# Performance work log

Measured on AMD Instinct MI355X. Metric: run time of the kernel, lower is better.

Reference implementation:

```python
import jax, jax.numpy as jnp
import numpy as np

D_MODEL = 1024
NUM_HEADS = 16
D_K = D_MODEL // NUM_HEADS


def setup_inputs() -> dict:
    key = jax.random.key(0)
    ks = jax.random.split(key, 11)
    B, S = 4, 2048
    s = 1.0 / np.sqrt(D_MODEL)
    return {
        "q": jax.random.normal(ks[0], (B, S, D_MODEL), jnp.float32),
        "k": jax.random.normal(ks[1], (B, S, D_MODEL), jnp.float32),
        "v": jax.random.normal(ks[2], (B, S, D_MODEL), jnp.float32),
        "w_q": jax.random.normal(ks[3], (D_MODEL, D_MODEL), jnp.float32) * s,
        "b_q": jnp.zeros((D_MODEL,), jnp.float32),
        "w_k": jax.random.normal(ks[4], (D_MODEL, D_MODEL), jnp.float32) * s,
        "b_k": jnp.zeros((D_MODEL,), jnp.float32),
        "w_v": jax.random.normal(ks[5], (D_MODEL, D_MODEL), jnp.float32) * s,
        "b_v": jnp.zeros((D_MODEL,), jnp.float32),
        "w_o": jax.random.normal(ks[6], (D_MODEL, D_MODEL), jnp.float32) * s,
        "b_o": jnp.zeros((D_MODEL,), jnp.float32),
    }


def reference(q, k, v, w_q, b_q, w_k, b_k, w_v, b_v, w_o, b_o):
    B, S, _ = q.shape
    # projections; torch Linear computes x @ W.T + b
    def proj(x, w, b):
        y = x @ w.T + b
        return y.reshape(B, -1, NUM_HEADS, D_K).transpose(0, 2, 1, 3)  # (B,H,S,d_k)

    qh, kh, vh = proj(q, w_q, b_q), proj(k, w_k, b_k), proj(v, w_v, b_v)
    scores = jnp.einsum("bhqd,bhkd->bhqk", qh, kh) / jnp.sqrt(jnp.float32(D_K))
    attn_weights = jax.nn.softmax(scores, axis=-1)
    x = jnp.einsum("bhqk,bhkd->bhqd", attn_weights, vh)
    x = x.transpose(0, 2, 1, 3).reshape(B, -1, D_MODEL)
    out = x @ w_o.T + b_o
    return out, attn_weights
```

## Files before the change

### kernel.cpp

```cpp
#include <hip/hip_runtime.h>
#include <math.h>

#define S_LEN 2048
#define DM 1024
#define NH 16
#define DK 64

typedef __attribute__((ext_vector_type(8))) short short8;
typedef __attribute__((ext_vector_type(4))) short short4v;
typedef __attribute__((ext_vector_type(4))) float f32x4;

#define LGKM_BARRIER() do { \
    asm volatile("s_waitcnt lgkmcnt(0)" ::: "memory"); \
    __builtin_amdgcn_s_barrier(); \
    __builtin_amdgcn_sched_barrier(0); \
  } while (0)

__device__ __forceinline__ short f2bf(float f) {
  unsigned u = __builtin_bit_cast(unsigned, f);
  u = (u + 0x7FFFu + ((u >> 16) & 1u)) >> 16;
  return (short)u;
}

__device__ __forceinline__ void gld_lds16(const short* g, short* l) {
  __builtin_amdgcn_global_load_lds(
      (const __attribute__((address_space(1))) unsigned int*)g,
      (__attribute__((address_space(3))) unsigned int*)l, 16, 0, 0);
}

__global__ __launch_bounds__(256) void cvt_bf16(
    const float* __restrict__ s0, const float* __restrict__ s1,
    const float* __restrict__ s2, const float* __restrict__ s3,
    short* __restrict__ d0, short* __restrict__ d1,
    short* __restrict__ d2, short* __restrict__ d3, int n)
{
  const float* s; short* d;
  switch (blockIdx.y) {
    case 0:  s = s0; d = d0; break;
    case 1:  s = s1; d = d1; break;
    case 2:  s = s2; d = d2; break;
    default: s = s3; d = d3; break;
  }
  const int i = (blockIdx.x * 256 + threadIdx.x) * 8;
  if (i < n) {
    const float4 v0 = *(const float4*)&s[i];
    const float4 v1 = *(const float4*)&s[i + 4];
    short8 r = { f2bf(v0.x), f2bf(v0.y), f2bf(v0.z), f2bf(v0.w),
                 f2bf(v1.x), f2bf(v1.y), f2bf(v1.z), f2bf(v1.w) };
    *(short8*)&d[i] = r;
  }
}

__global__ __launch_bounds__(256) void proj3(
    const short* __restrict__ qb, const short* __restrict__ kb, const short* __restrict__ vb,
    const short* __restrict__ wqb, const short* __restrict__ wkb, const short* __restrict__ wvb,
    const float* __restrict__ biq, const float* __restrict__ bik, const float* __restrict__ biv,
    short* __restrict__ qhb, short* __restrict__ khb, short* __restrict__ vtb)
{
  __shared__ short SM[17408];
  short* As = SM;
  short* Bs = SM + 4096;

  const int z = blockIdx.z;
  const short* A; const short* B; const float* bias; short* o;
  if (z == 0)      { A = qb; B = wqb; bias = biq; o = qhb; }
  else if (z == 1) { A = kb; B = wkb; bias = bik; o = khb; }
  else             { A = vb; B = wvb; bias = biv; o = vtb; }

  const int tid = threadIdx.x;
  const int lane = tid & 63;
  const int wv = tid >> 6;
  const int grp = lane >> 4, lid = lane & 15;
  const int wr = wv >> 1, wc = wv & 1;
  const int bm = blockIdx.x, bn = blockIdx.y;

  f32x4 acc[4][4] = {};

  const int idx0 = tid, idx1 = 256 + tid;
  const int r0 = idx0 >> 2, c0 = (idx0 & 3) * 8;
  const int r1 = idx1 >> 2, c1 = (idx1 & 3) * 8;
  const short* a0 = &A[(size_t)(bm * 128 + r0) * DM + c0];
  const short* a1 = &A[(size_t)(bm * 128 + r1) * DM + c1];
  const short* b0 = &B[(size_t)(bn * 128 + r0) * DM + c0];
  const short* b1 = &B[(size_t)(bn * 128 + r1) * DM + c1];

  for (int ks = 0; ks < 32; ++ks) {
    __syncthreads();
    gld_lds16(a0 + ks * 32, &As[idx0 * 8]);
    gld_lds16(a1 + ks * 32, &As[idx1 * 8]);
    gld_lds16(b0 + ks * 32, &Bs[idx0 * 8]);
    gld_lds16(b1 + ks * 32, &Bs[idx1 * 8]);
    __syncthreads();
    short8 a[4], b[4];
    #pragma unroll
    for (int m = 0; m < 4; ++m) a[m] = *(const short8*)&As[(wr * 64 + m * 16 + lid) * 32 + grp * 8];
    #pragma unroll
    for (int n = 0; n < 4; ++n) b[n] = *(const short8*)&Bs[(wc * 64 + n * 16 + lid) * 32 + grp * 8];
    #pragma unroll
    for (int m = 0; m < 4; ++m)
      #pragma unroll
      for (int n = 0; n < 4; ++n)
        acc[m][n] = __builtin_amdgcn_mfma_f32_16x16x32_bf16(a[m], b[n], acc[m][n], 0, 0, 0);
  }

  if (z < 2) {
    #pragma unroll
    for (int n = 0; n < 4; ++n) {
      const int ng = bn * 128 + wc * 64 + n * 16 + lid;
      const float bvs = bias[ng];
      const int h = ng >> 6, d = ng & 63;
      #pragma unroll
      for (int m = 0; m < 4; ++m) {
        const int mg = bm * 128 + wr * 64 + m * 16 + grp * 4;
        const int bb = mg >> 11, s = mg & 2047;
        #pragma unroll
        for (int r = 0; r < 4; ++r)
          o[(((size_t)bb * NH + h) * S_LEN + s + r) * DK + d] = f2bf(acc[m][n][r] + bvs);
      }
    }
  } else {
    __syncthreads();
    #pragma unroll
    for (int n = 0; n < 4; ++n) {
      const int ngl = wc * 64 + n * 16 + lid;
      const float bvs = bias[bn * 128 + ngl];
      #pragma unroll
      for (int m = 0; m < 4; ++m) {
        const int sl = wr * 64 + m * 16 + grp * 4;
        short4v c4 = { f2bf(acc[m][n][0] + bvs), f2bf(acc[m][n][1] + bvs),
                       f2bf(acc[m][n][2] + bvs), f2bf(acc[m][n][3] + bvs) };
        *(short4v*)&SM[ngl * 136 + sl] = c4;
      }
    }
    __syncthreads();
    const int bb = bm >> 4, s0 = (bm & 15) * 128;
    #pragma unroll
    for (int i = 0; i < 8; ++i) {
      const int id = tid + 256 * i;
      const int row = id >> 4;
      const int c8 = (id & 15) * 8;
      const short8 vv = *(const short8*)&SM[row * 136 + c8];
      *(short8*)&o[((size_t)bb * 1024 + bn * 128 + row) * S_LEN + s0 + c8] = vv;
    }
  }
}

__global__ __launch_bounds__(256) void gemm_o(
    const short* __restrict__ A, const short* __restrict__ B,
    const float* __restrict__ bias, float* __restrict__ of)
{
  __shared__ short As[128 * 32];
  __shared__ short Bs[128 * 32];
  const int tid = threadIdx.x;
  const int lane = tid & 63;
  const int wv = tid >> 6;
  const int grp = lane >> 4, lid = lane & 15;
  const int wr = wv >> 1, wc = wv & 1;
  const int bm = blockIdx.x, bn = blockIdx.y;

  f32x4 acc[4][4] = {};

  const int idx0 = tid, idx1 = 256 + tid;
  const int r0 = idx0 >> 2, c0 = (idx0 & 3) * 8;
  const int r1 = idx1 >> 2, c1 = (idx1 & 3) * 8;
  const short* a0 = &A[(size_t)(bm * 128 + r0) * DM + c0];
  const short* a1 = &A[(size_t)(bm * 128 + r1) * DM + c1];
  const short* b0 = &B[(size_t)(bn * 128 + r0) * DM + c0];
  const short* b1 = &B[(size_t)(bn * 128 + r1) * DM + c1];

  for (int ks = 0; ks < 32; ++ks) {
    __syncthreads();
    gld_lds16(a0 + ks * 32, &As[idx0 * 8]);
    gld_lds16(a1 + ks * 32, &As[idx1 * 8]);
    gld_lds16(b0 + ks * 32, &Bs[idx0 * 8]);
    gld_lds16(b1 + ks * 32, &Bs[idx1 * 8]);
    __syncthreads();
    short8 a[4], b[4];
    #pragma unroll
    for (int m = 0; m < 4; ++m) a[m] = *(const short8*)&As[(wr * 64 + m * 16 + lid) * 32 + grp * 8];
    #pragma unroll
    for (int n = 0; n < 4; ++n) b[n] = *(const short8*)&Bs[(wc * 64 + n * 16 + lid) * 32 + grp * 8];
    #pragma unroll
    for (int m = 0; m < 4; ++m)
      #pragma unroll
      for (int n = 0; n < 4; ++n)
        acc[m][n] = __builtin_amdgcn_mfma_f32_16x16x32_bf16(a[m], b[n], acc[m][n], 0, 0, 0);
  }

  #pragma unroll
  for (int n = 0; n < 4; ++n) {
    const int ng = bn * 128 + wc * 64 + n * 16 + lid;
    const float bvs = bias[ng];
    #pragma unroll
    for (int m = 0; m < 4; ++m) {
      const int mg = bm * 128 + wr * 64 + m * 16 + grp * 4;
      #pragma unroll
      for (int r = 0; r < 4; ++r)
        __builtin_nontemporal_store(acc[m][n][r] + bvs, &of[(size_t)(mg + r) * DM + ng]);
    }
  }
}

__global__ __launch_bounds__(128) void mha_attn10(
    const short* __restrict__ qh, const short* __restrict__ kh, const short* __restrict__ vt,
    float* __restrict__ attn, short* __restrict__ xb)
{
  __shared__ short Kt[64][72];
  __shared__ short Vt[64][72];
  __shared__ short Ps[2][32][72];

  const int tid = threadIdx.x;
  const int lane = tid & 63, wv = tid >> 6, grp = lane >> 4, lid = lane & 15;

  const int nid = blockIdx.x;
  const int x = nid & 7, jj = nid >> 3;
  const int bh = x + 8 * (jj >> 5);
  const int qt = jj & 31;

  const size_t baseQ = (size_t)bh * S_LEN * DK;
  const size_t baseV = (size_t)bh * DK * S_LEN;
  const float scale2 = 0.18033688f;

  const short* Qb = qh + baseQ;
  const short* Kb = kh + baseQ;
  const short* Vb = vt + baseV;

  int tr[4], tc[4];
  #pragma unroll
  for (int i = 0; i < 4; ++i) {
    const int id = tid + 128 * i;
    tr[i] = id >> 3; tc[i] = (id & 7) * 8;
  }

  short8 aq[2][2];
  #pragma unroll
  for (int qb2 = 0; qb2 < 2; ++qb2)
    #pragma unroll
    for (int kf = 0; kf < 2; ++kf)
      aq[qb2][kf] = *(const short8*)&Qb[(size_t)(qt * 64 + wv * 32 + qb2 * 16 + lid) * DK + kf * 32 + grp * 8];

  float lsum[2][4] = {};

  short8 kr[4];
  #pragma unroll
  for (int i = 0; i < 4; ++i) kr[i] = *(const short8*)&Kb[(size_t)tr[i] * DK + tc[i]];
  for (int kt = 0; kt < 32; ++kt) {
    short* buf = (kt & 1) ? &Ps[0][0][0] : &Kt[0][0];
    #pragma unroll
    for (int i = 0; i < 4; ++i) *(short8*)&buf[tr[i] * 72 + tc[i]] = kr[i];
    if (kt < 31) {
      #pragma unroll
      for (int i = 0; i < 4; ++i)
        kr[i] = *(const short8*)&Kb[(size_t)((kt + 1) * 64 + tr[i]) * DK + tc[i]];
    }
    LGKM_BARRIER();
    f32x4 sacc[4][2] = {};
    __builtin_amdgcn_s_setprio(1);
    #pragma unroll
    for (int kf = 0; kf < 2; ++kf) {
      short8 ak[4];
      #pragma unroll
      for (int kb2 = 0; kb2 < 4; ++kb2) ak[kb2] = *(const short8*)&buf[(kb2 * 16 + lid) * 72 + kf * 32 + grp * 8];
      #pragma unroll
      for (int kb2 = 0; kb2 < 4; ++kb2)
        #pragma unroll
        for (int qb2 = 0; qb2 < 2; ++qb2)
          sacc[kb2][qb2] = __builtin_amdgcn_mfma_f32_16x16x32_bf16(ak[kb2], aq[qb2][kf], sacc[kb2][qb2], 0, 0, 0);
    }
    __builtin_amdgcn_s_setprio(0);
    #pragma unroll
    for (int qb2 = 0; qb2 < 2; ++qb2)
      #pragma unroll
      for (int kb2 = 0; kb2 < 4; ++kb2) {
        float t0 = __builtin_amdgcn_exp2f(sacc[kb2][qb2][0] * scale2)
                 + __builtin_amdgcn_exp2f(sacc[kb2][qb2][1] * scale2);
        float t1 = __builtin_amdgcn_exp2f(sacc[kb2][qb2][2] * scale2)
                 + __builtin_amdgcn_exp2f(sacc[kb2][qb2][3] * scale2);
        lsum[qb2][kb2] += t0 + t1;
      }
  }

  float log2l[2];
  #pragma unroll
  for (int qb2 = 0; qb2 < 2; ++qb2) {
    float s = (lsum[qb2][0] + lsum[qb2][1]) + (lsum[qb2][2] + lsum[qb2][3]);
    s += __shfl_xor(s, 16);
    s += __shfl_xor(s, 32);
    log2l[qb2] = __log2f(s);
  }

  f32x4 oacc[2][4] = {};
  float* attnB = attn + ((size_t)bh * S_LEN + qt * 64 + wv * 32) * S_LEN;

  short8 vr[4];
  #pragma unroll
  for (int i = 0; i < 4; ++i) {
    kr[i] = *(const short8*)&Kb[(size_t)tr[i] * DK + tc[i]];
    vr[i] = *(const short8*)&Vb[(size_t)tr[i] * S_LEN + tc[i]];
  }
  for (int kt = 0; kt < 32; ++kt) {
    LGKM_BARRIER();
    #pragma unroll
    for (int i = 0; i < 4; ++i) {
      *(short8*)&Kt[tr[i]][tc[i]] = kr[i];
      *(short8*)&Vt[tr[i]][tc[i]] = vr[i];
    }
    if (kt < 31) {
      #pragma unroll
      for (int i = 0; i < 4; ++i) {
        kr[i] = *(const short8*)&Kb[(size_t)((kt + 1) * 64 + tr[i]) * DK + tc[i]];
        vr[i] = *(const short8*)&Vb[(size_t)tr[i] * S_LEN + (kt + 1) * 64 + tc[i]];
      }
    }
    LGKM_BARRIER();

    f32x4 sacc[4][2] = {};
    __builtin_amdgcn_s_setprio(1);
    #pragma unroll
    for (int kf = 0; kf < 2; ++kf) {
      short8 ak[4];
      #pragma unroll
      for (int kb2 = 0; kb2 < 4; ++kb2) ak[kb2] = *(const short8*)&Kt[kb2 * 16 + lid][kf * 32 + grp * 8];
      #pragma unroll
      for (int kb2 = 0; kb2 < 4; ++kb2)
        #pragma unroll
        for (int qb2 = 0; qb2 < 2; ++qb2)
          sacc[kb2][qb2] = __builtin_amdgcn_mfma_f32_16x16x32_bf16(ak[kb2], aq[qb2][kf], sacc[kb2][qb2], 0, 0, 0);
    }
    __builtin_amdgcn_s_setprio(0);

    #pragma unroll
    for (int qb2 = 0; qb2 < 2; ++qb2) {
      const float nl = -log2l[qb2];
      #pragma unroll
      for (int kb2 = 0; kb2 < 4; ++kb2) {
        short4v p4;
        #pragma unroll
        for (int r = 0; r < 4; ++r)
          p4[r] = f2bf(__builtin_amdgcn_exp2f(__builtin_fmaf(sacc[kb2][qb2][r], scale2, nl)));
        *(short4v*)&Ps[wv][qb2 * 16 + lid][kb2 * 16 + grp * 4] = p4;
      }
    }

    __builtin_amdgcn_s_setprio(1);
    #pragma unroll
    for (int kf = 0; kf < 2; ++kf) {
      short8 ap[2], bvv[4];
      #pragma unroll
      for (int mf = 0; mf < 2; ++mf) ap[mf] = *(const short8*)&Ps[wv][mf * 16 + lid][kf * 32 + grp * 8];
      #pragma unroll
      for (int nf = 0; nf < 4; ++nf) bvv[nf] = *(const short8*)&Vt[nf * 16 + lid][kf * 32 + grp * 8];
      #pragma unroll
      for (int mf = 0; mf < 2; ++mf)
        #pragma unroll
        for (int nf = 0; nf < 4; ++nf)
          oacc[mf][nf] = __builtin_amdgcn_mfma_f32_16x16x32_bf16(ap[mf], bvv[nf], oacc[mf][nf], 0, 0, 0);
    }
    __builtin_amdgcn_s_setprio(0);

    #pragma unroll
    for (int i = 0; i < 8; ++i) {
      const int qrow = i * 4 + grp;
      const uint2 u = *(const uint2*)&Ps[wv][qrow][lid * 4];
      f32x4 f;
      f[0] = __builtin_bit_cast(float, u.x << 16);
      f[1] = __builtin_bit_cast(float, u.x & 0xffff0000u);
      f[2] = __builtin_bit_cast(float, u.y << 16);
      f[3] = __builtin_bit_cast(float, u.y & 0xffff0000u);
      __builtin_nontemporal_store(f, (f32x4*)&attnB[(size_t)qrow * S_LEN + kt * 64 + lid * 4]);
    }
  }

  const int b = bh >> 4, h = bh & 15;
  #pragma unroll
  for (int mf = 0; mf < 2; ++mf) {
    #pragma unroll
    for (int nf = 0; nf < 4; ++nf) {
      #pragma unroll
      for (int r = 0; r < 4; ++r) {
        const int s = qt * 64 + wv * 32 + mf * 16 + grp * 4 + r;
        const int d = nf * 16 + lid;
        xb[((size_t)b * S_LEN + s) * DM + h * DK + d] = f2bf(oacc[mf][nf][r]);
      }
    }
  }
}

template<int MODE>
__global__ __launch_bounds__(256) void mha_gemm(
    const float* __restrict__ Af, const short* __restrict__ Ab,
    const float* __restrict__ W, const float* __restrict__ bias,
    short* __restrict__ obf, float* __restrict__ of)
{
  __shared__ short As[128][40];
  __shared__ short Bs[128][40];
  const int tid = threadIdx.x;
  const int lane = tid & 63, wv = tid >> 6;
  const int grp = lane >> 4, lid = lane & 15;
  const int wr = wv >> 1, wc = wv & 1;
  const int bm = blockIdx.x, bn = blockIdx.y;

  f32x4 acc[4][4] = {};

  for (int ks = 0; ks < 32; ++ks) {
    __syncthreads();
    if (MODE == 0) {
      #pragma unroll
      for (int i = 0; i < 4; ++i) {
        const int c = tid + 256 * i;
        const int row = c >> 3, kc = c & 7;
        const float4 v = *(const float4*)&Af[(size_t)(bm * 128 + row) * DM + ks * 32 + kc * 4];
        short4v s4 = { f2bf(v.x), f2bf(v.y), f2bf(v.z), f2bf(v.w) };
        *(short4v*)&As[row][kc * 4] = s4;
      }
    } else {
      #pragma unroll
      for (int i = 0; i < 2; ++i) {
        const int c = tid + 256 * i;
        const int row = c >> 2, k8 = (c & 3) * 8;
        *(float4*)&As[row][k8] = *(const float4*)&Ab[(size_t)(bm * 128 + row) * DM + ks * 32 + k8];
      }
    }
    #pragma unroll
    for (int i = 0; i < 4; ++i) {
      const int c = tid + 256 * i;
      const int row = c >> 3, kc = c & 7;
      const float4 v = *(const float4*)&W[(size_t)(bn * 128 + row) * DM + ks * 32 + kc * 4];
      short4v s4 = { f2bf(v.x), f2bf(v.y), f2bf(v.z), f2bf(v.w) };
      *(short4v*)&Bs[row][kc * 4] = s4;
    }
    __syncthreads();
    short8 a[4], b[4];
    #pragma unroll
    for (int m = 0; m < 4; ++m) a[m] = *(const short8*)&As[wr * 64 + m * 16 + lid][grp * 8];
    #pragma unroll
    for (int n = 0; n < 4; ++n) b[n] = *(const short8*)&Bs[wc * 64 + n * 16 + lid][grp * 8];
    #pragma unroll
    for (int m = 0; m < 4; ++m)
      #pragma unroll
      for (int n = 0; n < 4; ++n)
        acc[m][n] = __builtin_amdgcn_mfma_f32_16x16x32_bf16(a[m], b[n], acc[m][n], 0, 0, 0);
  }

  #pragma unroll
  for (int n = 0; n < 4; ++n) {
    const int ng = bn * 128 + wc * 64 + n * 16 + lid;
    const float bvs = bias[ng];
    #pragma unroll
    for (int m = 0; m < 4; ++m) {
      const int mg = bm * 128 + wr * 64 + m * 16 + grp * 4;
      #pragma unroll
      for (int r = 0; r < 4; ++r) {
        const float val = acc[m][n][r] + bvs;
        const int mm = mg + r;
        if (MODE == 0) {
          const int bb = mm >> 11, s = mm & 2047, h = ng >> 6, d = ng & 63;
          obf[(((size_t)bb * NH + h) * S_LEN + s) * DK + d] = f2bf(val);
        } else {
          of[(size_t)mm * DM + ng] = val;
        }
      }
    }
  }
}

__global__ __launch_bounds__(256) void mha_attn_old(
    const short* __restrict__ qh, const short* __restrict__ kh, const short* __restrict__ vh,
    float* __restrict__ attn, short* __restrict__ xb)
{
  __shared__ short QP[128][72];
  __shared__ short Ks[64][72];
  __shared__ short VT[64][72];

  const int tid = threadIdx.x;
  const int lane = tid & 63, wv = tid >> 6, grp = lane >> 4, lid = lane & 15;
  const int qt = blockIdx.x, bh = blockIdx.y;
  const size_t base = (size_t)bh * S_LEN * DK;
  const float scale = 0.125f;

  #pragma unroll
  for (int i = 0; i < 4; ++i) {
    const int c = tid + 256 * i;
    const int row = c >> 3, k8 = (c & 7) * 8;
    *(float4*)&QP[row][k8] = *(const float4*)&qh[base + (size_t)(qt * 128 + row) * DK + k8];
  }
  __syncthreads();
  short8 aq[2][2];
  #pragma unroll
  for (int mf = 0; mf < 2; ++mf)
    #pragma unroll
    for (int kf = 0; kf < 2; ++kf)
      aq[mf][kf] = *(const short8*)&QP[wv * 32 + mf * 16 + lid][kf * 32 + grp * 8];

  float lsum[2][4] = {};

  for (int kt = 0; kt < 32; ++kt) {
    __syncthreads();
    #pragma unroll
    for (int i = 0; i < 2; ++i) {
      const int c = tid + 256 * i;
      const int row = c >> 3, k8 = (c & 7) * 8;
      *(float4*)&Ks[row][k8] = *(const float4*)&kh[base + (size_t)(kt * 64 + row) * DK + k8];
    }
    __syncthreads();
    f32x4 sacc[2][4] = {};
    #pragma unroll
    for (int kf = 0; kf < 2; ++kf) {
      short8 bk[4];
      #pragma unroll
      for (int nf = 0; nf < 4; ++nf) bk[nf] = *(const short8*)&Ks[nf * 16 + lid][kf * 32 + grp * 8];
      #pragma unroll
      for (int mf = 0; mf < 2; ++mf)
        #pragma unroll
        for (int nf = 0; nf < 4; ++nf)
          sacc[mf][nf] = __builtin_amdgcn_mfma_f32_16x16x32_bf16(aq[mf][kf], bk[nf], sacc[mf][nf], 0, 0, 0);
    }
    #pragma unroll
    for (int mf = 0; mf < 2; ++mf)
      #pragma unroll
      for (int r = 0; r < 4; ++r)
        #pragma unroll
        for (int nf = 0; nf < 4; ++nf)
          lsum[mf][r] += __expf(sacc[mf][nf][r] * scale);
  }

  float rl[2][4];
  #pragma unroll
  for (int mf = 0; mf < 2; ++mf)
    #pragma unroll
    for (int r = 0; r < 4; ++r) {
      float s = lsum[mf][r];
      #pragma unroll
      for (int off = 8; off >= 1; off >>= 1) s += __shfl_xor(s, off, 16);
      rl[mf][r] = 1.f / s;
    }

  f32x4 oacc[2][4] = {};

  for (int kt = 0; kt < 32; ++kt) {
    __syncthreads();
    #pragma unroll
    for (int i = 0; i < 2; ++i) {
      const int c = tid + 256 * i;
      const int row = c >> 3, k8 = (c & 7) * 8;
      *(float4*)&Ks[row][k8] = *(const float4*)&kh[base + (size_t)(kt * 64 + row) * DK + k8];
    }
    #pragma unroll
    for (int i = 0; i < 2; ++i) {
      const int key = tid & 63;
      const int d0 = ((tid >> 6) << 3) + i * 32;
      const float4 v = *(const float4*)&vh[base + (size_t)(kt * 64 + key) * DK + d0];
      const short8 sv = __builtin_bit_cast(short8, v);
      #pragma unroll
      for (int jj = 0; jj < 8; ++jj) VT[d0 + jj][key] = sv[jj];
    }
    __syncthreads();
    f32x4 sacc[2][4] = {};
    #pragma unroll
    for (int kf = 0; kf < 2; ++kf) {
      short8 bk[4];
      #pragma unroll
      for (int nf = 0; nf < 4; ++nf) bk[nf] = *(const short8*)&Ks[nf * 16 + lid][kf * 32 + grp * 8];
      #pragma unroll
      for (int mf = 0; mf < 2; ++mf)
        #pragma unroll
        for (int nf = 0; nf < 4; ++nf)
          sacc[mf][nf] = __builtin_amdgcn_mfma_f32_16x16x32_bf16(aq[mf][kf], bk[nf], sacc[mf][nf], 0, 0, 0);
    }
    #pragma unroll
    for (int mf = 0; mf < 2; ++mf) {
      #pragma unroll
      for (int nf = 0; nf < 4; ++nf) {
        #pragma unroll
        for (int r = 0; r < 4; ++r) {
          const float p = __expf(sacc[mf][nf][r] * scale) * rl[mf][r];
          const int qr = wv * 32 + mf * 16 + grp * 4 + r;
          const int kc = kt * 64 + nf * 16 + lid;
          attn[((size_t)bh * S_LEN + qt * 128 + qr) * S_LEN + kc] = p;
          QP[wv * 32 + (qr & 31)][nf * 16 + lid] = f2bf(p);
        }
      }
    }
    #pragma unroll
    for (int kf = 0; kf < 2; ++kf) {
      short8 ap[2], bvv[4];
      #pragma unroll
      for (int mf = 0; mf < 2; ++mf) ap[mf] = *(const short8*)&QP[wv * 32 + mf * 16 + lid][kf * 32 + grp * 8];
      #pragma unroll
      for (int nf = 0; nf < 4; ++nf) bvv[nf] = *(const short8*)&VT[nf * 16 + lid][kf * 32 + grp * 8];
      #pragma unroll
      for (int mf = 0; mf < 2; ++mf)
        #pragma unroll
        for (int nf = 0; nf < 4; ++nf)
          oacc[mf][nf] = __builtin_amdgcn_mfma_f32_16x16x32_bf16(ap[mf], bvv[nf], oacc[mf][nf], 0, 0, 0);
    }
  }

  const int b = bh >> 4, h = bh & 15;
  #pragma unroll
  for (int mf = 0; mf < 2; ++mf) {
    #pragma unroll
    for (int nf = 0; nf < 4; ++nf) {
      #pragma unroll
      for (int r = 0; r < 4; ++r) {
        const int s = qt * 128 + wv * 32 + mf * 16 + grp * 4 + r;
        const int d = nf * 16 + lid;
        xb[((size_t)b * S_LEN + s) * DM + h * DK + d] = f2bf(oacc[mf][nf][r]);
      }
    }
  }
}

extern "C" void kernel_launch(void* const* d_in, const int* in_sizes, int n_in,
                              void* d_out, int out_size, void* d_ws, size_t ws_size,
                              hipStream_t stream) {
  const float* q  = (const float*)d_in[0];
  const float* k  = (const float*)d_in[1];
  const float* v  = (const float*)d_in[2];
  const float* wq = (const float*)d_in[3];
  const float* bq = (const float*)d_in[4];
  const float* wk = (const float*)d_in[5];
  const float* bk = (const float*)d_in[6];
  const float* wv = (const float*)d_in[7];
  const float* bv = (const float*)d_in[8];
  const float* wo = (const float*)d_in[9];
  const float* bo = (const float*)d_in[10];

  float* out  = (float*)d_out;
  float* attn = out + (size_t)4 * S_LEN * DM;

  const size_t NTOK = (size_t)4 * S_LEN * DM;
  const size_t NW   = (size_t)DM * DM;
  dim3 blk(256);

  if (ws_size >= 135000000ull) {
    short* qb  = (short*)d_ws;
    short* kb  = qb + NTOK;
    short* vb  = kb + NTOK;
    short* wqb = vb + NTOK;
    short* wkb = wqb + NW;
    short* wvb = wkb + NW;
    short* wob = wvb + NW;
    short* qhb = wob + NW;
    short* khb = qhb + NTOK;
    short* vtb = khb + NTOK;
    short* xb  = vtb + NTOK;

    cvt_bf16<<<dim3(4096, 3), blk, 0, stream>>>(q, k, v, (const float*)nullptr,
                                                qb, kb, vb, (short*)nullptr, (int)NTOK);
    cvt_bf16<<<dim3(512, 4), blk, 0, stream>>>(wq, wk, wv, wo, wqb, wkb, wvb, wob, (int)NW);

    proj3<<<dim3(64, 8, 3), blk, 0, stream>>>(qb, kb, vb, wqb, wkb, wvb, bq, bk, bv,
                                              qhb, khb, vtb);

    mha_attn10<<<dim3(2048), dim3(128), 0, stream>>>(qhb, khb, vtb, attn, xb);

    gemm_o<<<dim3(64, 8), blk, 0, stream>>>(xb, wob, bo, out);
  } else {
    short* qhb = (short*)d_ws;
    short* khb = qhb + NTOK;
    short* vhb = khb + NTOK;
    short* xb  = vhb + NTOK;

    mha_gemm<0><<<dim3(64, 8), blk, 0, stream>>>(q, (const short*)nullptr, wq, bq, qhb, (float*)nullptr);
    mha_gemm<0><<<dim3(64, 8), blk, 0, stream>>>(k, (const short*)nullptr, wk, bk, khb, (float*)nullptr);
    mha_gemm<0><<<dim3(64, 8), blk, 0, stream>>>(v, (const short*)nullptr, wv, bv, vhb, (float*)nullptr);
    mha_attn_old<<<dim3(16, 64), blk, 0, stream>>>(qhb, khb, vhb, attn, xb);
    mha_gemm<1><<<dim3(64, 8), blk, 0, stream>>>((const float*)nullptr, xb, wo, bo, (short*)nullptr, out);
  }
}
```

Baseline: 385.9 us.

## Double GEMM K-tile to 64 and store fp32 attention probs directly

The projection and output GEMMs now stage 64-wide K slices in LDS instead of 32, halving the number of barrier-separated load iterations and issuing two MFMA sub-steps per slice. The attention kernel writes fp32 softmax probabilities straight from registers rather than re-reading bf16 values from LDS and widening them. This removes the LDS round trip and gives the attention weights full fp32 precision, but the stores are now scattered by row-per-lane (16-byte chunks across rows), which may be less coalesced. The LDS footprint doubles for gemm_o, and proj3's B offset moves to fit within its existing buffer.

```diff
diff --git a/kernel.cpp b/kernel.cpp
--- a/kernel.cpp
+++ b/kernel.cpp
@@ -59,7 +59,7 @@
 {
   __shared__ short SM[17408];
   short* As = SM;
-  short* Bs = SM + 4096;
+  short* Bs = SM + 8192;
 
   const int z = blockIdx.z;
   const short* A; const short* B; const float* bias; short* o;
@@ -76,31 +76,37 @@
 
   f32x4 acc[4][4] = {};
 
-  const int idx0 = tid, idx1 = 256 + tid;
-  const int r0 = idx0 >> 2, c0 = (idx0 & 3) * 8;
-  const int r1 = idx1 >> 2, c1 = (idx1 & 3) * 8;
-  const short* a0 = &A[(size_t)(bm * 128 + r0) * DM + c0];
-  const short* a1 = &A[(size_t)(bm * 128 + r1) * DM + c1];
-  const short* b0 = &B[(size_t)(bn * 128 + r0) * DM + c0];
-  const short* b1 = &B[(size_t)(bn * 128 + r1) * DM + c1];
-
-  for (int ks = 0; ks < 32; ++ks) {
-    __syncthreads();
-    gld_lds16(a0 + ks * 32, &As[idx0 * 8]);
-    gld_lds16(a1 + ks * 32, &As[idx1 * 8]);
-    gld_lds16(b0 + ks * 32, &Bs[idx0 * 8]);
-    gld_lds16(b1 + ks * 32, &Bs[idx1 * 8]);
-    __syncthreads();
-    short8 a[4], b[4];
-    #pragma unroll
-    for (int m = 0; m < 4; ++m) a[m] = *(const short8*)&As[(wr * 64 + m * 16 + lid) * 32 + grp * 8];
-    #pragma unroll
-    for (int n = 0; n < 4; ++n) b[n] = *(const short8*)&Bs[(wc * 64 + n * 16 + lid) * 32 + grp * 8];
-    #pragma unroll
-    for (int m = 0; m < 4; ++m)
-      #pragma unroll
-      for (int n = 0; n < 4; ++n)
-        acc[m][n] = __builtin_amdgcn_mfma_f32_16x16x32_bf16(a[m], b[n], acc[m][n], 0, 0, 0);
+  const short* aP[4]; const short* bP[4]; int idxc[4];
+  #pragma unroll
+  for (int j = 0; j < 4; ++j) {
+    const int idx = tid + 256 * j;
+    idxc[j] = idx;
+    const int row = idx >> 3, c8 = (idx & 7) * 8;
+    aP[j] = &A[(size_t)(bm * 128 + row) * DM + c8];
+    bP[j] = &B[(size_t)(bn * 128 + row) * DM + c8];
+  }
+
+  for (int ks = 0; ks < 16; ++ks) {
+    __syncthreads();
+    #pragma unroll
+    for (int j = 0; j < 4; ++j) {
+      gld_lds16(aP[j] + ks * 64, &As[idxc[j] * 8]);
+      gld_lds16(bP[j] + ks * 64, &Bs[idxc[j] * 8]);
+    }
+    __syncthreads();
+    #pragma unroll
+    for (int kf = 0; kf < 2; ++kf) {
+      short8 a[4], b[4];
+      #pragma unroll
+      for (int m = 0; m < 4; ++m) a[m] = *(const short8*)&As[(wr * 64 + m * 16 + lid) * 64 + kf * 32 + grp * 8];
+      #pragma unroll
+      for (int n = 0; n < 4; ++n) b[n] = *(const short8*)&Bs[(wc * 64 + n * 16 + lid) * 64 + kf * 32 + grp * 8];
+      #pragma unroll
+      for (int m = 0; m < 4; ++m)
+        #pragma unroll
+        for (int n = 0; n < 4; ++n)
+          acc[m][n] = __builtin_amdgcn_mfma_f32_16x16x32_bf16(a[m], b[n], acc[m][n], 0, 0, 0);
+    }
   }
 
   if (z < 2) {
@@ -149,8 +155,8 @@
     const short* __restrict__ A, const short* __restrict__ B,
     const float* __restrict__ bias, float* __restrict__ of)
 {
-  __shared__ short As[128 * 32];
-  __shared__ short Bs[128 * 32];
+  __shared__ short As[128 * 64];
+  __shared__ short Bs[128 * 64];
   const int tid = threadIdx.x;
   const int lane = tid & 63;
   const int wv = tid >> 6;
@@ -160,31 +166,37 @@
 
   f32x4 acc[4][4] = {};
 
-  const int idx0 = tid, idx1 = 256 + tid;
-  const int r0 = idx0 >> 2, c0 = (idx0 & 3) * 8;
-  const int r1 = idx1 >> 2, c1 = (idx1 & 3) * 8;
-  const short* a0 = &A[(size_t)(bm * 128 + r0) * DM + c0];
-  const short* a1 = &A[(size_t)(bm * 128 + r1) * DM + c1];
-  const short* b0 = &B[(size_t)(bn * 128 + r0) * DM + c0];
-  const short* b1 = &B[(size_t)(bn * 128 + r1) * DM + c1];
-
-  for (int ks = 0; ks < 32; ++ks) {
-    __syncthreads();
-    gld_lds16(a0 + ks * 32, &As[idx0 * 8]);
-    gld_lds16(a1 + ks * 32, &As[idx1 * 8]);
-    gld_lds16(b0 + ks * 32, &Bs[idx0 * 8]);
-    gld_lds16(b1 + ks * 32, &Bs[idx1 * 8]);
-    __syncthreads();
-    short8 a[4], b[4];
-    #pragma unroll
-    for (int m = 0; m < 4; ++m) a[m] = *(const short8*)&As[(wr * 64 + m * 16 + lid) * 32 + grp * 8];
-    #pragma unroll
-    for (int n = 0; n < 4; ++n) b[n] = *(const short8*)&Bs[(wc * 64 + n * 16 + lid) * 32 + grp * 8];
-    #pragma unroll
-    for (int m = 0; m < 4; ++m)
-      #pragma unroll
-      for (int n = 0; n < 4; ++n)
-        acc[m][n] = __builtin_amdgcn_mfma_f32_16x16x32_bf16(a[m], b[n], acc[m][n], 0, 0, 0);
+  const short* aP[4]; const short* bP[4]; int idxc[4];
+  #pragma unroll
+  for (int j = 0; j < 4; ++j) {
+    const int idx = tid + 256 * j;
+    idxc[j] = idx;
+    const int row = idx >> 3, c8 = (idx & 7) * 8;
+    aP[j] = &A[(size_t)(bm * 128 + row) * DM + c8];
+    bP[j] = &B[(size_t)(bn * 128 + row) * DM + c8];
+  }
+
+  for (int ks = 0; ks < 16; ++ks) {
+    __syncthreads();
+    #pragma unroll
+    for (int j = 0; j < 4; ++j) {
+      gld_lds16(aP[j] + ks * 64, &As[idxc[j] * 8]);
+      gld_lds16(bP[j] + ks * 64, &Bs[idxc[j] * 8]);
+    }
+    __syncthreads();
+    #pragma unroll
+    for (int kf = 0; kf < 2; ++kf) {
+      short8 a[4], b[4];
+      #pragma unroll
+      for (int m = 0; m < 4; ++m) a[m] = *(const short8*)&As[(wr * 64 + m * 16 + lid) * 64 + kf * 32 + grp * 8];
+      #pragma unroll
+      for (int n = 0; n < 4; ++n) b[n] = *(const short8*)&Bs[(wc * 64 + n * 16 + lid) * 64 + kf * 32 + grp * 8];
+      #pragma unroll
+      for (int m = 0; m < 4; ++m)
+        #pragma unroll
+        for (int n = 0; n < 4; ++n)
+          acc[m][n] = __builtin_amdgcn_mfma_f32_16x16x32_bf16(a[m], b[n], acc[m][n], 0, 0, 0);
+    }
   }
 
   #pragma unroll
@@ -201,7 +213,7 @@
   }
 }
 
-__global__ __launch_bounds__(128) void mha_attn10(
+__global__ __launch_bounds__(128) void mha_attn11(
     const short* __restrict__ qh, const short* __restrict__ kh, const short* __restrict__ vt,
     float* __restrict__ attn, short* __restrict__ xb)
 {
@@ -332,12 +344,15 @@
     #pragma unroll
     for (int qb2 = 0; qb2 < 2; ++qb2) {
       const float nl = -log2l[qb2];
+      const size_t rowOff = (size_t)(qb2 * 16 + lid) * S_LEN + kt * 64;
       #pragma unroll
       for (int kb2 = 0; kb2 < 4; ++kb2) {
-        short4v p4;
+        f32x4 pf;
         #pragma unroll
         for (int r = 0; r < 4; ++r)
-          p4[r] = f2bf(__builtin_amdgcn_exp2f(__builtin_fmaf(sacc[kb2][qb2][r], scale2, nl)));
+          pf[r] = __builtin_amdgcn_exp2f(__builtin_fmaf(sacc[kb2][qb2][r], scale2, nl));
+        __builtin_nontemporal_store(pf, (f32x4*)&attnB[rowOff + kb2 * 16 + grp * 4]);
+        short4v p4 = { f2bf(pf[0]), f2bf(pf[1]), f2bf(pf[2]), f2bf(pf[3]) };
         *(short4v*)&Ps[wv][qb2 * 16 + lid][kb2 * 16 + grp * 4] = p4;
       }
     }
@@ -357,18 +372,6 @@
           oacc[mf][nf] = __builtin_amdgcn_mfma_f32_16x16x32_bf16(ap[mf], bvv[nf], oacc[mf][nf], 0, 0, 0);
     }
     __builtin_amdgcn_s_setprio(0);
-
-    #pragma unroll
-    for (int i = 0; i < 8; ++i) {
-      const int qrow = i * 4 + grp;
-      const uint2 u = *(const uint2*)&Ps[wv][qrow][lid * 4];
-      f32x4 f;
-      f[0] = __builtin_bit_cast(float, u.x << 16);
-      f[1] = __builtin_bit_cast(float, u.x & 0xffff0000u);
-      f[2] = __builtin_bit_cast(float, u.y << 16);
-      f[3] = __builtin_bit_cast(float, u.y & 0xffff0000u);
-      __builtin_nontemporal_store(f, (f32x4*)&attnB[(size_t)qrow * S_LEN + kt * 64 + lid * 4]);
-    }
   }
 
   const int b = bh >> 4, h = bh & 15;
@@ -653,7 +656,7 @@
     proj3<<<dim3(64, 8, 3), blk, 0, stream>>>(qb, kb, vb, wqb, wkb, wvb, bq, bk, bv,
                                               qhb, khb, vtb);
 
-    mha_attn10<<<dim3(2048), dim3(128), 0, stream>>>(qhb, khb, vtb, attn, xb);
+    mha_attn11<<<dim3(2048), dim3(128), 0, stream>>>(qhb, khb, vtb, attn, xb);
 
     gemm_o<<<dim3(64, 8), blk, 0, stream>>>(xb, wob, bo, out);
   } else {
```

After: 523.1 us. +35.5%, slower.
